# Kernel optimization log

Hardware: AMD Instinct MI355X
Metric: run time of the kernel (lower is better)

The kernel has to match this reference:

```python
import jax, jax.numpy as jnp
import numpy as np
from jax import lax

C = 64      # embed_dim
DI = 128    # d_inner (expand=2)
N = 16      # d_state
RK = 4      # dt_rank = ceil(C/16)
K = 4       # scan directions
NB = 8      # total VSS blocks (4 stages x 2)


def conv2d(x, w, b, stride=1, pad=1, groups=1):
    y = lax.conv_general_dilated(x, w, (stride, stride), [(pad, pad), (pad, pad)],
                                 dimension_numbers=('NCHW', 'OIHW', 'NCHW'),
                                 feature_group_count=groups)
    return y + b[None, :, None, None]


def ln2d(x, g, b, eps=1e-6):
    xt = x.transpose(0, 2, 3, 1)
    mu = xt.mean(-1, keepdims=True)
    var = ((xt - mu) ** 2).mean(-1, keepdims=True)
    y = (xt - mu) / jnp.sqrt(var + eps) * g + b
    return y.transpose(0, 3, 1, 2)


def selective_scan(u, delta, A, Bm, Cm, D):
    # u, delta: (B,K,d,L); A: (K,d,n); Bm, Cm: (B,K,n,L); D: (K,d)
    dA = jnp.exp(delta[..., None] * A[None, :, :, None, :])               # (B,K,d,L,n)
    dBu = delta[..., None] * Bm.transpose(0, 1, 3, 2)[:, :, None] * u[..., None]

    def comb(c1, c2):
        a1, b1 = c1
        a2, b2 = c2
        return a2 * a1, a2 * b1 + b2

    _, h = lax.associative_scan(comb, (dA, dBu), axis=3)                  # (B,K,d,L,n)
    y = jnp.einsum('bkdln,bkln->bkdl', h, Cm.transpose(0, 1, 3, 2))
    return y + D[None, :, :, None] * u


def vss_block(x, lg, lb, inw, cw, cb, xpw, dtw, dtb, a_log, dp, ong, onb, outw):
    B, _, H, W = x.shape
    L = H * W
    h = ln2d(x, lg, lb)
    xz = jnp.einsum('bchw,ce->behw', h, inw)                              # (B,2*DI,H,W)
    xc, z = xz[:, :DI], xz[:, DI:]
    xc = jax.nn.silu(conv2d(xc, cw, cb, groups=DI))                       # depthwise 3x3
    x1 = xc.reshape(B, DI, L)                                             # row-major
    x2 = xc.transpose(0, 1, 3, 2).reshape(B, DI, L)                       # col-major
    xs = jnp.stack([x1, x2, x1[..., ::-1], x2[..., ::-1]], axis=1)        # (B,K,DI,L)
    xdbl = jnp.einsum('bkdl,krd->bkrl', xs, xpw)
    dts, Bs, Cs = xdbl[:, :, :RK], xdbl[:, :, RK:RK + N], xdbl[:, :, RK + N:]
    delta = jax.nn.softplus(jnp.einsum('bkrl,kdr->bkdl', dts, dtw) + dtb[None, :, :, None])
    A = -jnp.exp(a_log)
    ys = selective_scan(xs, delta, A, Bs, Cs, dp)                         # (B,K,DI,L)
    y = (ys[:, 0].reshape(B, DI, H, W)
         + ys[:, 1].reshape(B, DI, W, H).transpose(0, 1, 3, 2)
         + ys[:, 2, :, ::-1].reshape(B, DI, H, W)
         + ys[:, 3, :, ::-1].reshape(B, DI, W, H).transpose(0, 1, 3, 2))
    yt = y.transpose(0, 2, 3, 1)
    mu = yt.mean(-1, keepdims=True)
    var = ((yt - mu) ** 2).mean(-1, keepdims=True)
    yt = (yt - mu) / jnp.sqrt(var + 1e-6) * ong + onb
    yt = yt * jax.nn.silu(z.transpose(0, 2, 3, 1))
    out = jnp.einsum('bhwd,dc->bhwc', yt, outw).transpose(0, 3, 1, 2)
    return x + out


def setup_inputs() -> dict:
    key = jax.random.key(0)
    ks = jax.random.split(key, 16)
    nrm = lambda k, s, sc=0.02: jax.random.normal(k, s, jnp.float32) * sc
    return dict(
        E0=jax.random.uniform(ks[0], (1, 1, 256, 256), jnp.float32),
        pe_w=nrm(ks[1], (C, 1, 4, 4), 0.1),
        pe_b=jnp.zeros((C,), jnp.float32),
        pe_lg=jnp.ones((C,), jnp.float32),
        pe_lb=jnp.zeros((C,), jnp.float32),
        ln_g=jnp.ones((NB, C), jnp.float32),
        ln_b=jnp.zeros((NB, C), jnp.float32),
        in_w=nrm(ks[2], (NB, C, 2 * DI)),
        cv_w=nrm(ks[3], (NB, DI, 1, 3, 3), 0.1),
        cv_b=jnp.zeros((NB, DI), jnp.float32),
        xp_w=nrm(ks[4], (NB, K, RK + 2 * N, DI)),
        dt_w=nrm(ks[5], (NB, K, DI, RK)),
        dt_b=nrm(ks[6], (NB, K, DI), 0.5),
        A_log=jnp.broadcast_to(jnp.log(jnp.arange(1., N + 1)), (NB, K, DI, N)).astype(jnp.float32),
        Dp=jnp.ones((NB, K, DI), jnp.float32),
        on_g=jnp.ones((NB, DI), jnp.float32),
        on_b=jnp.zeros((NB, DI), jnp.float32),
        out_pw=nrm(ks[7], (NB, DI, C)),
        dn_w=nrm(ks[8], (3, C, C, 3, 3), 0.05),
        dn_b=jnp.zeros((3, C), jnp.float32),
        dn_g=jnp.ones((3, C), jnp.float32),
        dn_lb=jnp.zeros((3, C), jnp.float32),
        up_w=nrm(ks[9], (3, C, C, 3, 3), 0.05),
        up_b=jnp.zeros((3, C), jnp.float32),
        oc_w=nrm(ks[10], (C, C, 3, 3), 0.05),
        oc_b=jnp.zeros((C,), jnp.float32),
    )


def reference(E0, pe_w, pe_b, pe_lg, pe_lb, ln_g, ln_b, in_w, cv_w, cv_b, xp_w,
              dt_w, dt_b, A_log, Dp, on_g, on_b, out_pw, dn_w, dn_b, dn_g, dn_lb,
              up_w, up_b, oc_w, oc_b):
    x = conv2d(E0, pe_w, pe_b, stride=4, pad=0)
    x = ln2d(x, pe_lg, pe_lb)
    skips = []
    cur = 0
    for i in range(4):
        for _ in range(2):
            x = vss_block(x, ln_g[cur], ln_b[cur], in_w[cur], cv_w[cur], cv_b[cur],
                          xp_w[cur], dt_w[cur], dt_b[cur], A_log[cur], Dp[cur],
                          on_g[cur], on_b[cur], out_pw[cur])
            cur += 1
        skips.append(x)
        if i < 3:
            x = ln2d(conv2d(x, dn_w[i], dn_b[i], stride=2), dn_g[i], dn_lb[i])
    for i in range(3):
        Bq, Cq, Hq, Wq = x.shape
        x = jax.image.resize(x, (Bq, Cq, Hq * 2, Wq * 2), method='bilinear')
        x = jax.nn.silu(conv2d(x, up_w[i], up_b[i]))
        x = x + skips[-(i + 2)]
    Bq, Cq, Hq, Wq = x.shape
    x = jax.image.resize(x, (Bq, Cq, Hq * 4, Wq * 4), method='bilinear')
    x = jax.nn.silu(conv2d(x, oc_w, oc_b))
    return x
```

## Files before the change

### kernel.cpp

```cpp
#include <hip/hip_runtime.h>
#include <hip/hip_bf16.h>
#include <utility>

__global__ void k_patch_embed_ln(const float* __restrict__ E0, const float* __restrict__ w,
                                 const float* __restrict__ b, const float* __restrict__ g,
                                 const float* __restrict__ lb, float* __restrict__ out) {
  int p = blockIdx.x;
  int c = threadIdx.x;
  int oh = p >> 6, ow = p & 63;
  const float* src = E0 + (oh * 4) * 256 + ow * 4;
  const float* wc = w + c * 16;
  float acc = b[c];
#pragma unroll
  for (int i = 0; i < 4; i++)
#pragma unroll
    for (int j = 0; j < 4; j++) acc += src[i * 256 + j] * wc[i * 4 + j];
  float s = acc, s2 = acc * acc;
#pragma unroll
  for (int m = 32; m >= 1; m >>= 1) {
    s += __shfl_xor(s, m, 64);
    s2 += __shfl_xor(s2, m, 64);
  }
  float mu = s * (1.f / 64.f);
  float var = s2 * (1.f / 64.f) - mu * mu;
  float rstd = rsqrtf(var + 1e-6f);
  out[c * 4096 + p] = (acc - mu) * rstd * g[c] + lb[c];
}

__global__ void k_ln2d64(const float* __restrict__ x, const float* __restrict__ g,
                         const float* __restrict__ b, float* __restrict__ y, int HW) {
  int p = blockIdx.x;
  int c = threadIdx.x;
  float v = x[c * HW + p];
  float s = v, s2 = v * v;
#pragma unroll
  for (int m = 32; m >= 1; m >>= 1) {
    s += __shfl_xor(s, m, 64);
    s2 += __shfl_xor(s2, m, 64);
  }
  float mu = s * (1.f / 64.f);
  float var = s2 * (1.f / 64.f) - mu * mu;
  float rstd = rsqrtf(var + 1e-6f);
  y[c * HW + p] = (v - mu) * rstd * g[c] + b[c];
}

__global__ void k_lnproj(const float* __restrict__ x, const float* __restrict__ g,
                         const float* __restrict__ b, const float* __restrict__ w,
                         float* __restrict__ xc, float* __restrict__ z, int HW) {
  int p = blockIdx.x;
  int t = threadIdx.x;
  __shared__ float hsh[64];
  if (t < 64) {
    float v = x[t * HW + p];
    float s = v, s2 = v * v;
#pragma unroll
    for (int m = 32; m >= 1; m >>= 1) {
      s += __shfl_xor(s, m, 64);
      s2 += __shfl_xor(s2, m, 64);
    }
    float mu = s * (1.f / 64.f);
    float var = s2 * (1.f / 64.f) - mu * mu;
    float rstd = rsqrtf(var + 1e-6f);
    hsh[t] = (v - mu) * rstd * g[t] + b[t];
  }
  __syncthreads();
  float acc = 0.f;
  const float* wp = w + t;
#pragma unroll
  for (int c = 0; c < 64; c++) acc += hsh[c] * wp[c * 256];
  if (t < 128)
    xc[(size_t)p * 128 + t] = acc;
  else
    z[(size_t)p * 128 + (t - 128)] = acc;
}

__global__ void k_dwconv(const float* __restrict__ xc, const float* __restrict__ w,
                         const float* __restrict__ b, float* __restrict__ out, int H, int lgH) {
  int HW = H * H;
  int idx = blockIdx.x * blockDim.x + threadIdx.x;
  if (idx >= 128 * HW) return;
  int p = idx >> 7;
  int d = idx & 127;
  int ph = p >> lgH, pw = p & (H - 1);
  const float* wp = w + d * 9;
  float acc = b[d];
#pragma unroll
  for (int i = 0; i < 3; i++) {
    int ih = ph + i - 1;
    if (ih < 0 || ih >= H) continue;
#pragma unroll
    for (int j = 0; j < 3; j++) {
      int iw = pw + j - 1;
      if (iw < 0 || iw >= H) continue;
      acc += xc[(size_t)(ih * H + iw) * 128 + d] * wp[i * 3 + j];
    }
  }
  out[(size_t)p * 128 + d] = acc / (1.f + __expf(-acc));
}

__global__ void __launch_bounds__(256) k_xproj_scanA(
    const float* __restrict__ xcs, const float* __restrict__ xpw,
    const float* __restrict__ dtw, const float* __restrict__ dtb,
    const float* __restrict__ A_log, float* __restrict__ delta, float* __restrict__ Bs,
    float* __restrict__ Cs, float* __restrict__ hloc, float* __restrict__ pA, int H,
    int lgH, int nc, int cs) {
  extern __shared__ float smem[];
  float* xs = smem;
  float* dsh = xs + cs * 128;
  float* Bsh = dsh + cs * 128;
  float* r4s = Bsh + cs * 16;
  int L = H * H;
  int c = blockIdx.x;
  int k = blockIdx.y;
  int t = threadIdx.x;
  int l0 = c * cs;
  for (int i = t; i < cs * 128; i += 256) {
    int j = i >> 7, d = i & 127;
    int l = l0 + j;
    int lm = (k & 2) ? (L - 1 - l) : l;
    int idx = (k & 1) ? ((lm & (H - 1)) * H + (lm >> lgH)) : lm;
    xs[j * 128 + d] = xcs[(size_t)idx * 128 + d];
  }
  int r = t >> 2, q = t & 3;
  float4 wreg[8];
  if (t < 144) {
    const float4* wp = (const float4*)(xpw + (size_t)(k * 36 + r) * 128 + q * 32);
#pragma unroll
    for (int m = 0; m < 8; m++) wreg[m] = wp[m];
  }
  float4 dtw4 = {0, 0, 0, 0};
  float dtbv = 0.f;
  if (t < 128) {
    dtw4 = *(const float4*)(dtw + (size_t)(k * 128 + t) * 4);
    dtbv = dtb[k * 128 + t];
  }
  __syncthreads();
  for (int j = 0; j < cs; j++) {
    if (t < 144) {
      const float4* xp = (const float4*)&xs[j * 128 + q * 32];
      float a = 0.f;
#pragma unroll
      for (int m = 0; m < 8; m++) {
        float4 xv = xp[m];
        a += xv.x * wreg[m].x + xv.y * wreg[m].y + xv.z * wreg[m].z + xv.w * wreg[m].w;
      }
      a += __shfl_xor(a, 1);
      a += __shfl_xor(a, 2);
      if (q == 0) {
        int l = l0 + j;
        if (r < 4)
          r4s[r] = a;
        else if (r < 20) {
          Bsh[j * 16 + (r - 4)] = a;
          Bs[((size_t)k * L + l) * 16 + (r - 4)] = a;
        } else
          Cs[((size_t)k * L + l) * 16 + (r - 20)] = a;
      }
    }
    __syncthreads();
    if (t < 128) {
      float dt = dtbv + r4s[0] * dtw4.x + r4s[1] * dtw4.y + r4s[2] * dtw4.z + r4s[3] * dtw4.w;
      float sp = fmaxf(dt, 0.f) + log1pf(__expf(-fabsf(dt)));
      dsh[j * 128 + t] = sp;
      delta[((size_t)k * L + (l0 + j)) * 128 + t] = sp;
    }
    __syncthreads();
  }
  if (t < 128) {
    int d = t;
    float A[16], h[16];
#pragma unroll
    for (int n = 0; n < 16; n++) {
      A[n] = -__expf(A_log[(size_t)(k * 128 + d) * 16 + n]);
      h[n] = 0.f;
    }
    float sumdt = 0.f;
    for (int j = 0; j < cs; j++) {
      float u = xs[j * 128 + d];
      float dt = dsh[j * 128 + d];
      float du = dt * u;
      sumdt += dt;
      const float4* bp = (const float4*)&Bsh[j * 16];
      float4 B0 = bp[0], B1 = bp[1], B2 = bp[2], B3 = bp[3];
      float Bv[16] = {B0.x, B0.y, B0.z, B0.w, B1.x, B1.y, B1.z, B1.w,
                      B2.x, B2.y, B2.z, B2.w, B3.x, B3.y, B3.z, B3.w};
#pragma unroll
      for (int n = 0; n < 16; n++) h[n] = __expf(dt * A[n]) * h[n] + Bv[n] * du;
    }
    size_t base = (((size_t)(k * 128 + d)) * nc + c) * 16;
#pragma unroll
    for (int n = 0; n < 16; n++) {
      hloc[base + n] = h[n];
      pA[base + n] = __expf(A[n] * sumdt);
    }
  }
}

__global__ void k_scanB(const float* __restrict__ hloc, const float* __restrict__ pA,
                        float* __restrict__ hinit, int nc) {
  int tid = blockIdx.x * blockDim.x + threadIdx.x;
  int k = tid >> 11;
  int d = (tid >> 4) & 127;
  int n = tid & 15;
  size_t rb = ((size_t)(k * 128 + d)) * nc * 16 + n;
  float h = 0.f;
  for (int c = 0; c < nc; c++) {
    size_t a = rb + (size_t)c * 16;
    hinit[a] = h;
    h = pA[a] * h + hloc[a];
  }
}

__global__ void k_scanC(const float* __restrict__ xcs, const float* __restrict__ delta,
                        const float* __restrict__ Bs, const float* __restrict__ Cs,
                        const float* __restrict__ A_log, const float* __restrict__ Dp,
                        const float* __restrict__ hinit, float* __restrict__ ys, int H,
                        int lgH, int nc, int cs) {
  int L = H * H;
  int c = blockIdx.x;
  int k = blockIdx.y;
  int d = threadIdx.x;
  float A[16], h[16];
  size_t base = (((size_t)(k * 128 + d)) * nc + c) * 16;
#pragma unroll
  for (int n = 0; n < 16; n++) {
    A[n] = -__expf(A_log[(size_t)(k * 128 + d) * 16 + n]);
    h[n] = hinit[base + n];
  }
  float Dv = Dp[k * 128 + d];
  int l0 = c * cs;
  for (int l = l0; l < l0 + cs; l++) {
    int lm = (k & 2) ? (L - 1 - l) : l;
    int idx = (k & 1) ? ((lm & (H - 1)) * H + (lm >> lgH)) : lm;
    float u = xcs[(size_t)idx * 128 + d];
    float dt = delta[((size_t)k * L + l) * 128 + d];
    float du = dt * u;
    const float4* bp = (const float4*)(Bs + ((size_t)k * L + l) * 16);
    float4 B0 = bp[0], B1 = bp[1], B2 = bp[2], B3 = bp[3];
    float Bv[16] = {B0.x, B0.y, B0.z, B0.w, B1.x, B1.y, B1.z, B1.w,
                    B2.x, B2.y, B2.z, B2.w, B3.x, B3.y, B3.z, B3.w};
    const float4* cp = (const float4*)(Cs + ((size_t)k * L + l) * 16);
    float4 C0 = cp[0], C1 = cp[1], C2 = cp[2], C3 = cp[3];
    float Cv[16] = {C0.x, C0.y, C0.z, C0.w, C1.x, C1.y, C1.z, C1.w,
                    C2.x, C2.y, C2.z, C2.w, C3.x, C3.y, C3.z, C3.w};
    float y = 0.f;
#pragma unroll
    for (int n = 0; n < 16; n++) {
      h[n] = __expf(dt * A[n]) * h[n] + Bv[n] * du;
      y += h[n] * Cv[n];
    }
    ys[((size_t)k * L + l) * 128 + d] = y + Dv * u;
  }
}

__global__ void k_combine(const float* __restrict__ ys, const float* __restrict__ z,
                          const float* __restrict__ xin, const float* __restrict__ ong,
                          const float* __restrict__ onb, const float* __restrict__ outw,
                          float* __restrict__ xout, int H, int lgH) {
  int L = H * H;
  int p = blockIdx.x;
  int d = threadIdx.x;
  int ph = p >> lgH, pw = p & (H - 1);
  int l1 = pw * H + ph;
  float yv = ys[((size_t)0 * L + p) * 128 + d] + ys[((size_t)1 * L + l1) * 128 + d] +
             ys[((size_t)2 * L + (L - 1 - p)) * 128 + d] +
             ys[((size_t)3 * L + (L - 1 - l1)) * 128 + d];
  float s = yv, s2 = yv * yv;
#pragma unroll
  for (int m = 32; m >= 1; m >>= 1) {
    s += __shfl_xor(s, m, 64);
    s2 += __shfl_xor(s2, m, 64);
  }
  __shared__ float ws1[2], ws2[2];
  int wid = d >> 6;
  if ((d & 63) == 0) {
    ws1[wid] = s;
    ws2[wid] = s2;
  }
  __syncthreads();
  float tot = ws1[0] + ws1[1], tot2 = ws2[0] + ws2[1];
  float mu = tot * (1.f / 128.f);
  float var = tot2 * (1.f / 128.f) - mu * mu;
  float rstd = rsqrtf(var + 1e-6f);
  float zt = z[(size_t)p * 128 + d];
  float yt = ((yv - mu) * rstd * ong[d] + onb[d]) * (zt / (1.f + __expf(-zt)));
  __shared__ float ysm[128];
  ysm[d] = yt;
  __syncthreads();
  if (d < 64) {
    float acc = xin[(size_t)d * L + p];
#pragma unroll
    for (int q = 0; q < 128; q++) acc += ysm[q] * outw[q * 64 + d];
    xout[(size_t)d * L + p] = acc;
  }
}

__global__ void k_combine_lnproj(const float* __restrict__ ys, const float* __restrict__ z,
                                 const float* __restrict__ xin, const float* __restrict__ ong,
                                 const float* __restrict__ onb, const float* __restrict__ outw,
                                 const float* __restrict__ g2, const float* __restrict__ b2,
                                 const float* __restrict__ w2, float* __restrict__ xout,
                                 float* __restrict__ xc, float* __restrict__ zout, int H,
                                 int lgH) {
  int L = H * H;
  int p = blockIdx.x;
  int t = threadIdx.x;
  __shared__ float ysm[128], hnsh[64];
  __shared__ float ws1[2], ws2[2];
  float yv = 0.f;
  if (t < 128) {
    int ph = p >> lgH, pw = p & (H - 1);
    int l1 = pw * H + ph;
    yv = ys[((size_t)0 * L + p) * 128 + t] + ys[((size_t)1 * L + l1) * 128 + t] +
         ys[((size_t)2 * L + (L - 1 - p)) * 128 + t] +
         ys[((size_t)3 * L + (L - 1 - l1)) * 128 + t];
    float s = yv, s2 = yv * yv;
#pragma unroll
    for (int m = 32; m >= 1; m >>= 1) {
      s += __shfl_xor(s, m, 64);
      s2 += __shfl_xor(s2, m, 64);
    }
    if ((t & 63) == 0) {
      ws1[t >> 6] = s;
      ws2[t >> 6] = s2;
    }
  }
  __syncthreads();
  if (t < 128) {
    float tot = ws1[0] + ws1[1], tot2 = ws2[0] + ws2[1];
    float mu = tot * (1.f / 128.f);
    float var = tot2 * (1.f / 128.f) - mu * mu;
    float rstd = rsqrtf(var + 1e-6f);
    float zt = z[(size_t)p * 128 + t];
    ysm[t] = ((yv - mu) * rstd * ong[t] + onb[t]) * (zt / (1.f + __expf(-zt)));
  }
  __syncthreads();
  if (t < 64) {
    float acc = xin[(size_t)t * L + p];
#pragma unroll
    for (int q = 0; q < 128; q++) acc += ysm[q] * outw[q * 64 + t];
    xout[(size_t)t * L + p] = acc;
    float s = acc, s2 = acc * acc;
#pragma unroll
    for (int m = 32; m >= 1; m >>= 1) {
      s += __shfl_xor(s, m, 64);
      s2 += __shfl_xor(s2, m, 64);
    }
    float mu = s * (1.f / 64.f);
    float var = s2 * (1.f / 64.f) - mu * mu;
    float rstd = rsqrtf(var + 1e-6f);
    hnsh[t] = (acc - mu) * rstd * g2[t] + b2[t];
  }
  __syncthreads();
  float a2 = 0.f;
  const float* wp = w2 + t;
#pragma unroll
  for (int c = 0; c < 64; c++) a2 += hnsh[c] * wp[c * 256];
  if (t < 128)
    xc[(size_t)p * 128 + t] = a2;
  else
    zout[(size_t)p * 128 + (t - 128)] = a2;
}

__global__ void k_conv_naive(const float* __restrict__ x, const float* __restrict__ w,
                             const float* __restrict__ b, const float* __restrict__ skip,
                             float* __restrict__ out, int Hin, int Hout, int stride,
                             int do_silu) {
  int idx = blockIdx.x * blockDim.x + threadIdx.x;
  int HWo = Hout * Hout;
  if (idx >= 64 * HWo) return;
  int co = idx / HWo;
  int p = idx - co * HWo;
  int oh = p / Hout, ow = p - (p / Hout) * Hout;
  float acc = b[co];
  const float* wb = w + co * 64 * 9;
  for (int ci = 0; ci < 64; ci++) {
    const float* xb = x + (size_t)ci * Hin * Hin;
    const float* wc = wb + ci * 9;
#pragma unroll
    for (int i = 0; i < 3; i++) {
      int ih = oh * stride + i - 1;
      if (ih < 0 || ih >= Hin) continue;
#pragma unroll
      for (int j = 0; j < 3; j++) {
        int iw = ow * stride + j - 1;
        if (iw < 0 || iw >= Hin) continue;
        acc += xb[ih * Hin + iw] * wc[i * 3 + j];
      }
    }
  }
  if (do_silu) acc = acc / (1.f + __expf(-acc));
  if (skip) acc += skip[idx];
  out[idx] = acc;
}

__global__ void k_phase_weights(const float* __restrict__ w, float* __restrict__ Wp) {
  int co = blockIdx.x;
  int ph = blockIdx.y;
  int ci = threadIdx.x;
  int py = ph >> 2, px = ph & 3;
  float ay[3][3], ax[3][3];
#pragma unroll
  for (int d = 0; d < 3; d++)
#pragma unroll
    for (int s = 0; s < 3; s++) {
      ay[d][s] = 0.f;
      ax[d][s] = 0.f;
    }
#pragma unroll
  for (int d = 0; d < 3; d++) {
    {
      float tt = (py + d - 1) * 0.25f - 0.375f;
      float e = floorf(tt);
      float f = tt - e;
      int ei = (int)e;
#pragma unroll
      for (int s = 0; s < 3; s++) {
        if (s == ei + 1) ay[d][s] += 1.f - f;
        if (s == ei + 2) ay[d][s] += f;
      }
    }
    {
      float tt = (px + d - 1) * 0.25f - 0.375f;
      float e = floorf(tt);
      float f = tt - e;
      int ei = (int)e;
#pragma unroll
      for (int s = 0; s < 3; s++) {
        if (s == ei + 1) ax[d][s] += 1.f - f;
        if (s == ei + 2) ax[d][s] += f;
      }
    }
  }
  const float* wc = w + ((size_t)co * 64 + ci) * 9;
  float wv[9];
#pragma unroll
  for (int i = 0; i < 9; i++) wv[i] = wc[i];
  float* dst = Wp + (((size_t)ph * 64 + co) * 64 + ci) * 9;
#pragma unroll
  for (int sy = 0; sy < 3; sy++)
#pragma unroll
    for (int sx = 0; sx < 3; sx++) {
      float a = 0.f;
#pragma unroll
      for (int dy = 0; dy < 3; dy++)
#pragma unroll
        for (int dx = 0; dx < 3; dx++) a += wv[dy * 3 + dx] * ay[dy][sy] * ax[dx][sx];
      dst[sy * 3 + sx] = a;
    }
}

__global__ void __launch_bounds__(256) k_conv_phase(const float* __restrict__ x,
                                                    const float* __restrict__ Wp,
                                                    const float* __restrict__ bias,
                                                    float* __restrict__ out) {
  __shared__ __align__(16) float ssh[8][18][20];
  __shared__ __align__(16) float wsh[8][16][12];
  int t = threadIdx.x;
  int q = t & 63, cg = t >> 6;
  int qx = q & 7, qy = q >> 3;
  int tx = blockIdx.x & 3, ty = blockIdx.x >> 2;
  int ph = blockIdx.y;
  int py = ph >> 2, px = ph & 3;
  int z16 = blockIdx.z * 16;
  int by = ty * 16, bx = tx * 16;
  float acc[4][4];
#pragma unroll
  for (int pp = 0; pp < 4; pp++)
#pragma unroll
    for (int i = 0; i < 4; i++) acc[pp][i] = 0.f;
  for (int cb = 0; cb < 64; cb += 8) {
    for (int i = t; i < 8 * 324; i += 256) {
      int ci = i / 324;
      int rr = i - ci * 324;
      int ry = rr / 18, rx = rr - ry * 18;
      int sy = min(max(by + ry - 1, 0), 63);
      int sx = min(max(bx + rx - 1, 0), 63);
      ssh[ci][ry][rx] = x[(size_t)(cb + ci) * 4096 + sy * 64 + sx];
    }
    for (int i = t; i < 8 * 144; i += 256) {
      int ci = i / 144;
      int rr = i - ci * 144;
      int col = rr / 9, tap = rr - col * 9;
      wsh[ci][col][tap] = Wp[(((size_t)ph * 64 + z16 + col) * 64 + cb + ci) * 9 + tap];
    }
    __syncthreads();
#pragma unroll 2
    for (int ci = 0; ci < 8; ci++) {
      float xv[4][4];
#pragma unroll
      for (int r = 0; r < 4; r++) {
        float2 a = *(const float2*)&ssh[ci][2 * qy + r][2 * qx];
        float2 bq = *(const float2*)&ssh[ci][2 * qy + r][2 * qx + 2];
        xv[r][0] = a.x;
        xv[r][1] = a.y;
        xv[r][2] = bq.x;
        xv[r][3] = bq.y;
      }
#pragma unroll
      for (int i = 0; i < 4; i++) {
        int col = cg * 4 + i;
        float4 w0 = *(const float4*)&wsh[ci][col][0];
        float4 w1 = *(const float4*)&wsh[ci][col][4];
        float w8 = wsh[ci][col][8];
#pragma unroll
        for (int dr = 0; dr < 2; dr++)
#pragma unroll
          for (int dc = 0; dc < 2; dc++) {
            acc[dr * 2 + dc][i] += xv[dr + 0][dc + 0] * w0.x + xv[dr + 0][dc + 1] * w0.y +
                                   xv[dr + 0][dc + 2] * w0.z + xv[dr + 1][dc + 0] * w0.w +
                                   xv[dr + 1][dc + 1] * w1.x + xv[dr + 1][dc + 2] * w1.y +
                                   xv[dr + 2][dc + 0] * w1.z + xv[dr + 2][dc + 1] * w1.w +
                                   xv[dr + 2][dc + 2] * w8;
          }
      }
    }
    __syncthreads();
  }
#pragma unroll
  for (int dr = 0; dr < 2; dr++)
#pragma unroll
    for (int dc = 0; dc < 2; dc++) {
      int sy = by + 2 * qy + dr, sx = bx + 2 * qx + dc;
      int gy = 4 * sy + py, gx = 4 * sx + px;
#pragma unroll
      for (int i = 0; i < 4; i++) {
        int co = z16 + cg * 4 + i;
        float a = acc[dr * 2 + dc][i] + bias[co];
        a = a / (1.f + __expf(-a));
        out[(size_t)co * 65536 + gy * 256 + gx] = a;
      }
    }
}

__global__ void k_final_ring(const float* __restrict__ x, const float* __restrict__ w,
                             const float* __restrict__ b, float* __restrict__ out) {
  int tid = blockIdx.x * blockDim.x + threadIdx.x;
  if (tid >= 1020 * 64) return;
  int co = tid & 63;
  int pix = tid >> 6;
  int gy, gx;
  if (pix < 256) {
    gy = 0;
    gx = pix;
  } else if (pix < 512) {
    gy = 255;
    gx = pix - 256;
  } else if (pix < 766) {
    gy = pix - 512 + 1;
    gx = 0;
  } else {
    gy = pix - 766 + 1;
    gx = 255;
  }
  float fh[3], fw[3];
  int y0[3], y1[3], x0[3], x1[3];
  bool vy[3], vx[3];
#pragma unroll
  for (int d = 0; d < 3; d++) {
    int g = gy + d - 1;
    vy[d] = (g >= 0 && g < 256);
    float s = g * 0.25f - 0.375f;
    float e = floorf(s);
    int ei = (int)e;
    fh[d] = s - e;
    y0[d] = min(max(ei, 0), 63);
    y1[d] = min(max(ei + 1, 0), 63);
    g = gx + d - 1;
    vx[d] = (g >= 0 && g < 256);
    s = g * 0.25f - 0.375f;
    e = floorf(s);
    ei = (int)e;
    fw[d] = s - e;
    x0[d] = min(max(ei, 0), 63);
    x1[d] = min(max(ei + 1, 0), 63);
  }
  const float* wb = w + (size_t)co * 576;
  float acc = b[co];
  for (int ci = 0; ci < 64; ci++) {
    const float* xb = x + (size_t)ci * 4096;
    const float* wc = wb + ci * 9;
#pragma unroll
    for (int dy = 0; dy < 3; dy++) {
      if (!vy[dy]) continue;
#pragma unroll
      for (int dx = 0; dx < 3; dx++) {
        if (!vx[dx]) continue;
        float u = (1.f - fh[dy]) * ((1.f - fw[dx]) * xb[y0[dy] * 64 + x0[dx]] +
                                    fw[dx] * xb[y0[dy] * 64 + x1[dx]]) +
                  fh[dy] * ((1.f - fw[dx]) * xb[y1[dy] * 64 + x0[dx]] +
                            fw[dx] * xb[y1[dy] * 64 + x1[dx]]);
        acc += wc[dy * 3 + dx] * u;
      }
    }
  }
  acc = acc / (1.f + __expf(-acc));
  out[(size_t)co * 65536 + gy * 256 + gx] = acc;
}

__global__ void k_resize(const float* __restrict__ x, float* __restrict__ out, int Hin,
                         int Win, int Hout, int Wout, float inv_scale) {
  int idx = blockIdx.x * blockDim.x + threadIdx.x;
  int HWo = Hout * Wout;
  if (idx >= 64 * HWo) return;
  int c = idx / HWo;
  int p = idx - c * HWo;
  int oh = p / Wout, ow = p - (p / Wout) * Wout;
  float sh = (oh + 0.5f) * inv_scale - 0.5f;
  float sw = (ow + 0.5f) * inv_scale - 0.5f;
  int h0 = (int)floorf(sh);
  float fh = sh - h0;
  int w0 = (int)floorf(sw);
  float fw = sw - w0;
  int h0c = min(max(h0, 0), Hin - 1), h1c = min(max(h0 + 1, 0), Hin - 1);
  int w0c = min(max(w0, 0), Win - 1), w1c = min(max(w0 + 1, 0), Win - 1);
  const float* xb = x + (size_t)c * Hin * Win;
  float v = (1.f - fh) * ((1.f - fw) * xb[h0c * Win + w0c] + fw * xb[h0c * Win + w1c]) +
            fh * ((1.f - fw) * xb[h1c * Win + w0c] + fw * xb[h1c * Win + w1c]);
  out[idx] = v;
}

extern "C" void kernel_launch(void* const* d_in, const int* in_sizes, int n_in, void* d_out,
                              int out_size, void* d_ws, size_t ws_size, hipStream_t stream) {
  const float* E0 = (const float*)d_in[0];
  const float* pe_w = (const float*)d_in[1];
  const float* pe_b = (const float*)d_in[2];
  const float* pe_lg = (const float*)d_in[3];
  const float* pe_lb = (const float*)d_in[4];
  const float* ln_g = (const float*)d_in[5];
  const float* ln_b = (const float*)d_in[6];
  const float* in_w = (const float*)d_in[7];
  const float* cv_w = (const float*)d_in[8];
  const float* cv_b = (const float*)d_in[9];
  const float* xp_w = (const float*)d_in[10];
  const float* dt_w = (const float*)d_in[11];
  const float* dt_b = (const float*)d_in[12];
  const float* A_log = (const float*)d_in[13];
  const float* Dp = (const float*)d_in[14];
  const float* on_g = (const float*)d_in[15];
  const float* on_b = (const float*)d_in[16];
  const float* out_pw = (const float*)d_in[17];
  const float* dn_w = (const float*)d_in[18];
  const float* dn_b = (const float*)d_in[19];
  const float* dn_g = (const float*)d_in[20];
  const float* dn_lb = (const float*)d_in[21];
  const float* up_w = (const float*)d_in[22];
  const float* up_b = (const float*)d_in[23];
  const float* oc_w = (const float*)d_in[24];
  const float* oc_b = (const float*)d_in[25];

  float* ws = (float*)d_ws;
  size_t off = 0;
  auto alloc = [&](size_t n) {
    float* p = ws + off;
    off += n;
    return p;
  };
  float* xA = alloc(64 * 4096);
  float* xB = alloc(64 * 4096);
  float* xc = alloc(128 * 4096);
  float* zb = alloc(128 * 4096);
  float* xcs = alloc(128 * 4096);
  float* dlt = alloc((size_t)4 * 128 * 4096);
  float* Bsb = alloc(4 * 16 * 4096);
  float* Csb = alloc(4 * 16 * 4096);
  float* ysb = alloc((size_t)4 * 128 * 4096);
  float* hloc = alloc((size_t)4 * 128 * 256 * 16);
  float* pAb = alloc((size_t)4 * 128 * 256 * 16);
  float* hin = alloc((size_t)4 * 128 * 256 * 16);
  float* sk0 = alloc(64 * 4096);
  float* sk1 = alloc(64 * 1024);
  float* sk2 = alloc(64 * 256);
  float* sk3 = alloc(64 * 64);
  float* tmpR = alloc((size_t)64 * 4096);
  float* Wpb = alloc((size_t)16 * 64 * 64 * 9);

  k_phase_weights<<<dim3(64, 16), 64, 0, stream>>>(oc_w, Wpb);

  k_patch_embed_ln<<<4096, 64, 0, stream>>>(E0, pe_w, pe_b, pe_lg, pe_lb, xB);
  float* x = xB;
  float* xalt = xA;

  int Hs[4] = {64, 32, 16, 8};
  int lgHs[4] = {6, 5, 4, 3};
  int CSs[4] = {16, 16, 8, 8};
  float* skips[4] = {sk0, sk1, sk2, sk3};
  int cur = 0;

  auto vss_core = [&](int H, int lgH, int cs) {
    int L = H * H;
    int nc = L / cs;
    k_dwconv<<<(128 * L + 255) / 256, 256, 0, stream>>>(xc, cv_w + (size_t)cur * 128 * 9,
                                                        cv_b + cur * 128, xcs, H, lgH);
    const float* Al = A_log + (size_t)cur * 4 * 128 * 16;
    const float* Dv = Dp + cur * 4 * 128;
    dim3 ga(nc, 4);
    size_t shb = (size_t)(cs * 128 * 2 + cs * 16 + 4) * sizeof(float);
    k_xproj_scanA<<<ga, 256, shb, stream>>>(xcs, xp_w + (size_t)cur * 4 * 36 * 128,
                                            dt_w + (size_t)cur * 4 * 128 * 4,
                                            dt_b + cur * 4 * 128, Al, dlt, Bsb, Csb, hloc,
                                            pAb, H, lgH, nc, cs);
    k_scanB<<<32, 256, 0, stream>>>(hloc, pAb, hin, nc);
    dim3 gc(nc, 4);
    k_scanC<<<gc, 128, 0, stream>>>(xcs, dlt, Bsb, Csb, Al, Dv, hin, ysb, H, lgH, nc, cs);
  };

  for (int i = 0; i < 4; i++) {
    int H = Hs[i], lgH = lgHs[i];
    int L = H * H;
    k_lnproj<<<L, 256, 0, stream>>>(x, ln_g + cur * 64, ln_b + cur * 64,
                                    in_w + (size_t)cur * 64 * 256, xc, zb, L);
    vss_core(H, lgH, CSs[i]);
    k_combine_lnproj<<<L, 256, 0, stream>>>(
        ysb, zb, x, on_g + cur * 128, on_b + cur * 128, out_pw + (size_t)cur * 128 * 64,
        ln_g + (cur + 1) * 64, ln_b + (cur + 1) * 64, in_w + (size_t)(cur + 1) * 64 * 256,
        xalt, xc, zb, H, lgH);
    std::swap(x, xalt);
    cur++;
    vss_core(H, lgH, CSs[i]);
    if (i < 3) {
      k_combine<<<L, 128, 0, stream>>>(ysb, zb, x, on_g + cur * 128, on_b + cur * 128,
                                       out_pw + (size_t)cur * 128 * 64, skips[i], H, lgH);
      cur++;
      int Ho = H / 2;
      k_conv_naive<<<(64 * Ho * Ho + 255) / 256, 256, 0, stream>>>(
          skips[i], dn_w + (size_t)i * 64 * 64 * 9, dn_b + i * 64, nullptr, xalt, H, Ho, 2, 0);
      k_ln2d64<<<Ho * Ho, 64, 0, stream>>>(xalt, dn_g + i * 64, dn_lb + i * 64, x, Ho * Ho);
    } else {
      k_combine<<<L, 128, 0, stream>>>(ysb, zb, x, on_g + cur * 128, on_b + cur * 128,
                                       out_pw + (size_t)cur * 128 * 64, xalt, H, lgH);
      std::swap(x, xalt);
      cur++;
    }
  }

  for (int i = 0; i < 3; i++) {
    int Hin = 8 << i, Ho = Hin * 2;
    k_resize<<<(64 * Ho * Ho + 255) / 256, 256, 0, stream>>>(x, tmpR, Hin, Hin, Ho, Ho, 0.5f);
    k_conv_naive<<<(64 * Ho * Ho + 255) / 256, 256, 0, stream>>>(
        tmpR, up_w + (size_t)i * 64 * 64 * 9, up_b + i * 64, skips[2 - i], xalt, Ho, Ho, 1, 1);
    std::swap(x, xalt);
  }

  dim3 gp(16, 16, 4);
  k_conv_phase<<<gp, 256, 0, stream>>>(x, Wpb, oc_b, (float*)d_out);
  k_final_ring<<<255, 256, 0, stream>>>(x, oc_w, oc_b, (float*)d_out);
}
```

Baseline: 1.278 ms.

## Vectorize dwconv, inline chunk-prefix scan for small stages, enlarge stage-0 chunks

The depthwise conv now has each thread handle four channels, using float4 loads and stores, so it launches a quarter as many threads. When a stage has 32 or fewer chunks, scanC computes its own chunk prefix state sequentially from hloc/pA, which skips the scanB launch. Stage 0 uses 32-element chunks, halving the number of chunks and shrinking the hloc, pA and hin buffers. The risk is redundant prefix work in later chunks and less parallelism in the stage-0 scan.

```diff
diff --git a/kernel.cpp b/kernel.cpp
--- a/kernel.cpp
+++ b/kernel.cpp
@@ -78,12 +78,11 @@
                          const float* __restrict__ b, float* __restrict__ out, int H, int lgH) {
   int HW = H * H;
   int idx = blockIdx.x * blockDim.x + threadIdx.x;
-  if (idx >= 128 * HW) return;
-  int p = idx >> 7;
-  int d = idx & 127;
+  if (idx >= 32 * HW) return;
+  int p = idx >> 5;
+  int d0 = (idx & 31) * 4;
   int ph = p >> lgH, pw = p & (H - 1);
-  const float* wp = w + d * 9;
-  float acc = b[d];
+  float4 acc = *(const float4*)(b + d0);
 #pragma unroll
   for (int i = 0; i < 3; i++) {
     int ih = ph + i - 1;
@@ -92,10 +91,20 @@
     for (int j = 0; j < 3; j++) {
       int iw = pw + j - 1;
       if (iw < 0 || iw >= H) continue;
-      acc += xc[(size_t)(ih * H + iw) * 128 + d] * wp[i * 3 + j];
-    }
-  }
-  out[(size_t)p * 128 + d] = acc / (1.f + __expf(-acc));
+      float4 xv = *(const float4*)(xc + (size_t)(ih * H + iw) * 128 + d0);
+      int tap = i * 3 + j;
+      acc.x += xv.x * w[(d0 + 0) * 9 + tap];
+      acc.y += xv.y * w[(d0 + 1) * 9 + tap];
+      acc.z += xv.z * w[(d0 + 2) * 9 + tap];
+      acc.w += xv.w * w[(d0 + 3) * 9 + tap];
+    }
+  }
+  float4 o;
+  o.x = acc.x / (1.f + __expf(-acc.x));
+  o.y = acc.y / (1.f + __expf(-acc.y));
+  o.z = acc.z / (1.f + __expf(-acc.z));
+  o.w = acc.w / (1.f + __expf(-acc.w));
+  *(float4*)(out + (size_t)p * 128 + d0) = o;
 }
 
 __global__ void __launch_bounds__(256) k_xproj_scanA(
@@ -214,18 +223,37 @@
 __global__ void k_scanC(const float* __restrict__ xcs, const float* __restrict__ delta,
                         const float* __restrict__ Bs, const float* __restrict__ Cs,
                         const float* __restrict__ A_log, const float* __restrict__ Dp,
+                        const float* __restrict__ hloc, const float* __restrict__ pA,
                         const float* __restrict__ hinit, float* __restrict__ ys, int H,
-                        int lgH, int nc, int cs) {
+                        int lgH, int nc, int cs, int ipref) {
   int L = H * H;
   int c = blockIdx.x;
   int k = blockIdx.y;
   int d = threadIdx.x;
   float A[16], h[16];
-  size_t base = (((size_t)(k * 128 + d)) * nc + c) * 16;
-#pragma unroll
-  for (int n = 0; n < 16; n++) {
-    A[n] = -__expf(A_log[(size_t)(k * 128 + d) * 16 + n]);
-    h[n] = hinit[base + n];
+  size_t rb = ((size_t)(k * 128 + d)) * nc * 16;
+#pragma unroll
+  for (int n = 0; n < 16; n++) A[n] = -__expf(A_log[(size_t)(k * 128 + d) * 16 + n]);
+  if (ipref) {
+#pragma unroll
+    for (int n = 0; n < 16; n++) h[n] = 0.f;
+    for (int cc = 0; cc < c; cc++) {
+      const float4* pp = (const float4*)(pA + rb + (size_t)cc * 16);
+      const float4* hh = (const float4*)(hloc + rb + (size_t)cc * 16);
+      float4 P0 = pp[0], P1 = pp[1], P2 = pp[2], P3 = pp[3];
+      float4 Q0 = hh[0], Q1 = hh[1], Q2 = hh[2], Q3 = hh[3];
+      h[0] = P0.x * h[0] + Q0.x;  h[1] = P0.y * h[1] + Q0.y;
+      h[2] = P0.z * h[2] + Q0.z;  h[3] = P0.w * h[3] + Q0.w;
+      h[4] = P1.x * h[4] + Q1.x;  h[5] = P1.y * h[5] + Q1.y;
+      h[6] = P1.z * h[6] + Q1.z;  h[7] = P1.w * h[7] + Q1.w;
+      h[8] = P2.x * h[8] + Q2.x;  h[9] = P2.y * h[9] + Q2.y;
+      h[10] = P2.z * h[10] + Q2.z; h[11] = P2.w * h[11] + Q2.w;
+      h[12] = P3.x * h[12] + Q3.x; h[13] = P3.y * h[13] + Q3.y;
+      h[14] = P3.z * h[14] + Q3.z; h[15] = P3.w * h[15] + Q3.w;
+    }
+  } else {
+#pragma unroll
+    for (int n = 0; n < 16; n++) h[n] = hinit[rb + (size_t)c * 16 + n];
   }
   float Dv = Dp[k * 128 + d];
   int l0 = c * cs;
@@ -665,9 +693,9 @@
   float* Bsb = alloc(4 * 16 * 4096);
   float* Csb = alloc(4 * 16 * 4096);
   float* ysb = alloc((size_t)4 * 128 * 4096);
-  float* hloc = alloc((size_t)4 * 128 * 256 * 16);
-  float* pAb = alloc((size_t)4 * 128 * 256 * 16);
-  float* hin = alloc((size_t)4 * 128 * 256 * 16);
+  float* hloc = alloc((size_t)4 * 128 * 128 * 16);
+  float* pAb = alloc((size_t)4 * 128 * 128 * 16);
+  float* hin = alloc((size_t)4 * 128 * 128 * 16);
   float* sk0 = alloc(64 * 4096);
   float* sk1 = alloc(64 * 1024);
   float* sk2 = alloc(64 * 256);
@@ -683,15 +711,15 @@
 
   int Hs[4] = {64, 32, 16, 8};
   int lgHs[4] = {6, 5, 4, 3};
-  int CSs[4] = {16, 16, 8, 8};
+  int CSs[4] = {32, 16, 8, 8};
   float* skips[4] = {sk0, sk1, sk2, sk3};
   int cur = 0;
 
   auto vss_core = [&](int H, int lgH, int cs) {
     int L = H * H;
     int nc = L / cs;
-    k_dwconv<<<(128 * L + 255) / 256, 256, 0, stream>>>(xc, cv_w + (size_t)cur * 128 * 9,
-                                                        cv_b + cur * 128, xcs, H, lgH);
+    k_dwconv<<<(32 * L + 255) / 256, 256, 0, stream>>>(xc, cv_w + (size_t)cur * 128 * 9,
+                                                       cv_b + cur * 128, xcs, H, lgH);
     const float* Al = A_log + (size_t)cur * 4 * 128 * 16;
     const float* Dv = Dp + cur * 4 * 128;
     dim3 ga(nc, 4);
@@ -700,9 +728,11 @@
                                             dt_w + (size_t)cur * 4 * 128 * 4,
                                             dt_b + cur * 4 * 128, Al, dlt, Bsb, Csb, hloc,
                                             pAb, H, lgH, nc, cs);
-    k_scanB<<<32, 256, 0, stream>>>(hloc, pAb, hin, nc);
+    int ipref = (nc <= 32) ? 1 : 0;
+    if (!ipref) k_scanB<<<32, 256, 0, stream>>>(hloc, pAb, hin, nc);
     dim3 gc(nc, 4);
-    k_scanC<<<gc, 128, 0, stream>>>(xcs, dlt, Bsb, Csb, Al, Dv, hin, ysb, H, lgH, nc, cs);
+    k_scanC<<<gc, 128, 0, stream>>>(xcs, dlt, Bsb, Csb, Al, Dv, hloc, pAb, hin, ysb, H,
+                                    lgH, nc, cs, ipref);
   };
 
   for (int i = 0; i < 4; i++) {
```

Measured after the change: 1.306 ms. 1.02x slower.
